# Kernel tuning notes

Hardware: AMD Instinct MI355X
Metric: run time of the kernel (lower is better)

The kernel has to match this reference:

```python
import jax, jax.numpy as jnp
import numpy as np

N_HEADS = 16
WINDOW = 256


def setup_inputs() -> dict:
    key = jax.random.key(0)
    ks = jax.random.split(key, 6)
    B, S, D = 2, 2048, 1024
    std = 0.02
    x = jax.random.normal(ks[0], (B, S, D), dtype=jnp.float32)
    wq = jax.random.normal(ks[1], (D, D), dtype=jnp.float32) * std
    wk = jax.random.normal(ks[2], (D, D), dtype=jnp.float32) * std
    wv = jax.random.normal(ks[3], (D, D), dtype=jnp.float32) * std
    wo = jax.random.normal(ks[4], (D, D), dtype=jnp.float32) * std
    bq = jnp.zeros((D,), jnp.float32)
    bk = jnp.zeros((D,), jnp.float32)
    bv = jnp.zeros((D,), jnp.float32)
    bo = jnp.zeros((D,), jnp.float32)
    return {"x": x, "wq": wq, "bq": bq, "wk": wk, "bk": bk,
            "wv": wv, "bv": bv, "wo": wo, "bo": bo}


def _sliding_window_bias(seq_len: int) -> jnp.ndarray:
    # allowed iff |i - j| <= WINDOW  ->  0.0, else -inf  (matches torch loop mask)
    i = jnp.arange(seq_len)[:, None]
    j = jnp.arange(seq_len)[None, :]
    allowed = jnp.abs(i - j) <= WINDOW
    return jnp.where(allowed, 0.0, -jnp.inf).astype(jnp.float32)


def reference(x, wq, bq, wk, bk, wv, bv, wo, bo):
    B, S, D = x.shape
    H = N_HEADS
    dh = D // H
    scale = dh ** -0.5
    # nn.Linear: y = x @ W^T + b
    q = (x @ wq.T + bq).reshape(B, S, H, dh).transpose(0, 2, 1, 3)  # [B,H,S,dh]
    k = (x @ wk.T + bk).reshape(B, S, H, dh).transpose(0, 2, 1, 3)
    v = (x @ wv.T + bv).reshape(B, S, H, dh).transpose(0, 2, 1, 3)
    scores = jnp.einsum('bhqd,bhkd->bhqk', q, k) * scale  # [B,H,S,S]
    scores = scores + _sliding_window_bias(S)[None, None]
    attn = jax.nn.softmax(scores, axis=-1)
    out = jnp.einsum('bhqk,bhkd->bhqd', attn, v)  # [B,H,S,dh]
    out = out.transpose(0, 2, 1, 3).reshape(B, S, D)
    return out @ wo.T + bo
```

## Files before the change

kernel.cpp:

```cpp
#include <hip/hip_runtime.h>
#include <stdint.h>

static constexpr int Ss = 2048;
static constexpr int Dd = 1024;
static constexpr int Hh = 16;
static constexpr int DH = 64;

typedef short bf16x8 __attribute__((ext_vector_type(8)));
typedef float f32x4 __attribute__((ext_vector_type(4)));

#define LOG2E 1.4426950408889634f

__device__ __forceinline__ uint16_t f2bf(float f) {
  uint32_t u = __builtin_bit_cast(uint32_t, f);
  u += 0x7fffu + ((u >> 16) & 1u);
  return (uint16_t)(u >> 16);
}
__device__ __forceinline__ float bf2f(uint16_t h) {
  uint32_t u = ((uint32_t)h) << 16;
  return __builtin_bit_cast(float, u);
}

template <int CTRL>
__device__ __forceinline__ float dppf(float x) {
  return __builtin_bit_cast(float,
      __builtin_amdgcn_update_dpp(0, __builtin_bit_cast(int, x), CTRL, 0xF, 0xF, true));
}
__device__ __forceinline__ float rowmax16(float v) {
  v = fmaxf(v, dppf<0x128>(v));
  v = fmaxf(v, dppf<0x124>(v));
  v = fmaxf(v, dppf<0x122>(v));
  v = fmaxf(v, dppf<0x121>(v));
  return v;
}
__device__ __forceinline__ float rowsum16(float v) {
  v += dppf<0x128>(v);
  v += dppf<0x124>(v);
  v += dppf<0x122>(v);
  v += dppf<0x121>(v);
  return v;
}
__device__ __forceinline__ float fexp2(float x) { return __builtin_amdgcn_exp2f(x); }

#define GAS(p) ((const __attribute__((address_space(1))) uint32_t*)(p))
#define LAS(p) ((__attribute__((address_space(3))) uint32_t*)(p))

__global__ void cvt_all(const float* __restrict__ x,
                        const float* __restrict__ w0, const float* __restrict__ w1,
                        const float* __restrict__ w2, const float* __restrict__ w3,
                        uint16_t* __restrict__ xb,
                        uint16_t* __restrict__ o0, uint16_t* __restrict__ o1,
                        uint16_t* __restrict__ o2, uint16_t* __restrict__ o3) {
  int bid = blockIdx.x;
  const float* in;
  uint16_t* out;
  int i;
  if (bid < 4096) {
    in = x; out = xb; i = bid * 256 + threadIdx.x;
  } else {
    int b2 = bid - 4096;
    int t = b2 >> 10;
    in = (t == 0) ? w0 : (t == 1) ? w1 : (t == 2) ? w2 : w3;
    out = (t == 0) ? o0 : (t == 1) ? o1 : (t == 2) ? o2 : o3;
    i = (b2 & 1023) * 256 + threadIdx.x;
  }
  float4 v = reinterpret_cast<const float4*>(in)[i];
  ushort4 o;
  o.x = f2bf(v.x); o.y = f2bf(v.y); o.z = f2bf(v.z); o.w = f2bf(v.w);
  reinterpret_cast<ushort4*>(out)[i] = o;
}

template <int MODE, int BN>
__global__ __launch_bounds__(256, 2) void gemm_nt(
    const uint16_t* __restrict__ A,
    const uint16_t* __restrict__ W0, const uint16_t* __restrict__ W1, const uint16_t* __restrict__ W2,
    const float* __restrict__ b0, const float* __restrict__ b1, const float* __restrict__ b2,
    void* __restrict__ O0, void* __restrict__ O1, void* __restrict__ O2,
    int M, int N, int K) {
  constexpr int NI = BN / 32;
  __shared__ __align__(16) uint8_t ldsA[128 * 128];
  __shared__ __align__(16) uint8_t ldsB[BN * 128];

  const int tid = threadIdx.x, w = tid >> 6, lane = tid & 63;
  const int q = lane & 15, g = lane >> 4;
  const int wm = w >> 1, wn = w & 1;
  const int bx = blockIdx.x, by = blockIdx.y, z = blockIdx.z;
  const uint16_t* Wp = (z == 0) ? W0 : (z == 1) ? W1 : W2;
  const float* bp = (z == 0) ? b0 : (z == 1) ? b1 : b2;
  void* Op = (z == 0) ? O0 : (z == 1) ? O1 : O2;

  f32x4 acc[4][NI] = {};

  const int nkt = K >> 6;
  for (int kt = 0; kt < nkt; ++kt) {
    const int k0 = kt << 6;
    __syncthreads();
#pragma unroll
    for (int i = 0; i < 4; ++i) {
      int Lb = w * 4096 + i * 1024 + lane * 16;
      int row = Lb >> 7, cb = Lb & 127;
      int col = (cb ^ ((row & 7) << 4)) >> 1;
      const uint16_t* srcA = A + (size_t)(bx * 128 + row) * K + k0 + col;
      __builtin_amdgcn_global_load_lds(GAS(srcA), LAS(ldsA + w * 4096 + i * 1024), 16, 0, 0);
    }
#pragma unroll
    for (int i = 0; i < BN / 32; ++i) {
      int Lb = w * (BN * 32) + i * 1024 + lane * 16;
      int row = Lb >> 7, cb = Lb & 127;
      int col = (cb ^ ((row & 7) << 4)) >> 1;
      const uint16_t* srcB = Wp + (size_t)(by * BN + row) * K + k0 + col;
      __builtin_amdgcn_global_load_lds(GAS(srcB), LAS(ldsB + w * (BN * 32) + i * 1024), 16, 0, 0);
    }
    __syncthreads();

    bf16x8 af[4][2], bfg[NI][2];
#pragma unroll
    for (int mi = 0; mi < 4; ++mi)
#pragma unroll
      for (int s = 0; s < 2; ++s) {
        int row = wm * 64 + mi * 16 + q;
        int cb = (16 * g + 64 * s) ^ ((row & 7) << 4);
        af[mi][s] = *(const bf16x8*)(ldsA + row * 128 + cb);
      }
#pragma unroll
    for (int ni = 0; ni < NI; ++ni)
#pragma unroll
      for (int s = 0; s < 2; ++s) {
        int row = wn * (BN / 2) + ni * 16 + q;
        int cb = (16 * g + 64 * s) ^ ((row & 7) << 4);
        bfg[ni][s] = *(const bf16x8*)(ldsB + row * 128 + cb);
      }
#pragma unroll
    for (int mi = 0; mi < 4; ++mi)
#pragma unroll
      for (int ni = 0; ni < NI; ++ni) {
        acc[mi][ni] = __builtin_amdgcn_mfma_f32_16x16x32_bf16(af[mi][0], bfg[ni][0], acc[mi][ni], 0, 0, 0);
        acc[mi][ni] = __builtin_amdgcn_mfma_f32_16x16x32_bf16(af[mi][1], bfg[ni][1], acc[mi][ni], 0, 0, 0);
      }
  }

  float bias[NI];
#pragma unroll
  for (int ni = 0; ni < NI; ++ni) bias[ni] = bp[by * BN + wn * (BN / 2) + ni * 16 + q];
#pragma unroll
  for (int mi = 0; mi < 4; ++mi)
#pragma unroll
    for (int ni = 0; ni < NI; ++ni)
#pragma unroll
      for (int r = 0; r < 4; ++r) {
        int m = bx * 128 + wm * 64 + mi * 16 + 4 * g + r;
        int n = by * BN + wn * (BN / 2) + ni * 16 + q;
        float v = acc[mi][ni][r] + bias[ni];
        if (MODE == 0) {
          int b = m >> 11, s = m & 2047, h = n >> 6, d = n & 63;
          ((uint16_t*)Op)[(((size_t)(b * Hh + h) * Ss + s) << 6) + d] = f2bf(v);
        } else {
          ((float*)Op)[(size_t)m * N + n] = v;
        }
      }
}

__global__ __launch_bounds__(256, 4) void attn_swa(
    const uint16_t* __restrict__ Qg, const uint16_t* __restrict__ Kg,
    const uint16_t* __restrict__ Vg, uint16_t* __restrict__ Og) {
  __shared__ __align__(16) uint8_t ldsK[2][64 * 128];
  __shared__ __align__(16) uint8_t ldsVt[2][64 * 128];
  __shared__ __align__(16) uint8_t ldsP[4][2048];

  const int tid = threadIdx.x, w = tid >> 6, lane = tid & 63;
  const int q = lane & 15, g = lane >> 4;
  const int qb = blockIdx.x, bh = blockIdx.y;
  const size_t hbase = (size_t)bh * Ss * DH;
  const uint16_t* Qp = Qg + hbase;
  const uint16_t* Kp = Kg + hbase;
  const uint16_t* Vp = Vg + hbase;
  const int q0 = qb * 64;
  const int qw = q0 + w * 16;

  bf16x8 aq[2];
#pragma unroll
  for (int s = 0; s < 2; ++s) {
    bf16x8 t = *(const bf16x8*)(Qp + (size_t)(qw + q) * DH + s * 32 + g * 8);
#pragma unroll
    for (int j = 0; j < 8; ++j) {
      float f = bf2f((uint16_t)t[j]) * 0.125f;
      t[j] = (short)f2bf(f);
    }
    aq[s] = t;
  }

  f32x4 accO[4] = {};
  float mrun[4] = {-1e30f, -1e30f, -1e30f, -1e30f};
  float lrun[4] = {0.f, 0.f, 0.f, 0.f};

  const int t0 = (q0 >= 256) ? (q0 - 256) : 0;
  const int t1 = (q0 + 320 <= Ss) ? (q0 + 320) : Ss;
  const int nt = (t1 - t0) >> 6;

#pragma unroll
  for (int i = 0; i < 2; ++i) {
    int Lb = w * 2048 + i * 1024 + lane * 16;
    int row = Lb >> 7, cb = Lb & 127;
    const uint16_t* srcK = Kp + (size_t)(t0 + row) * DH + ((cb ^ ((row & 7) << 4)) >> 1);
    __builtin_amdgcn_global_load_lds(GAS(srcK), LAS(ldsK[0] + w * 2048 + i * 1024), 16, 0, 0);
  }
  const uint16_t* vrow0 = Vp + (size_t)(t0 + lane) * DH + w * 16;
  bf16x8 v0 = *(const bf16x8*)(vrow0);
  bf16x8 v1 = *(const bf16x8*)(vrow0 + 8);

  for (int t = 0; t < nt; ++t) {
    const int kb0 = t0 + (t << 6);
    const int cur = t & 1, nxt = cur ^ 1;

    uint8_t* Vt = ldsVt[cur];
#pragma unroll
    for (int j = 0; j < 8; ++j) {
      int c0 = w * 16 + j;
      *(uint16_t*)(Vt + c0 * 128 + ((2 * lane) ^ ((c0 & 7) << 4))) = (uint16_t)v0[j];
      int c1 = w * 16 + 8 + j;
      *(uint16_t*)(Vt + c1 * 128 + ((2 * lane) ^ ((c1 & 7) << 4))) = (uint16_t)v1[j];
    }
    asm volatile("s_waitcnt lgkmcnt(0)" ::: "memory");
    __builtin_amdgcn_sched_barrier(0);
    __builtin_amdgcn_s_barrier();
    __builtin_amdgcn_sched_barrier(0);

    if (t + 1 < nt) {
#pragma unroll
      for (int i = 0; i < 2; ++i) {
        int Lb = w * 2048 + i * 1024 + lane * 16;
        int row = Lb >> 7, cb = Lb & 127;
        const uint16_t* srcK = Kp + (size_t)(kb0 + 64 + row) * DH + ((cb ^ ((row & 7) << 4)) >> 1);
        __builtin_amdgcn_global_load_lds(GAS(srcK), LAS(ldsK[nxt] + w * 2048 + i * 1024), 16, 0, 0);
      }
      const uint16_t* vrow = Vp + (size_t)(kb0 + 64 + lane) * DH + w * 16;
      v0 = *(const bf16x8*)(vrow);
      v1 = *(const bf16x8*)(vrow + 8);
    }

    const uint8_t* Kl = ldsK[cur];
    f32x4 sacc[4] = {};
#pragma unroll
    for (int kb = 0; kb < 4; ++kb) {
      int row = kb * 16 + q;
#pragma unroll
      for (int s = 0; s < 2; ++s) {
        int cb = (16 * g + 64 * s) ^ ((row & 7) << 4);
        bf16x8 bk = *(const bf16x8*)(Kl + row * 128 + cb);
        sacc[kb] = __builtin_amdgcn_mfma_f32_16x16x32_bf16(aq[s], bk, sacc[kb], 0, 0, 0);
      }
    }
    if (kb0 - q0 < -192 || kb0 - q0 > 192) {
#pragma unroll
      for (int kb = 0; kb < 4; ++kb) {
        int key = kb0 + kb * 16 + q;
#pragma unroll
        for (int r = 0; r < 4; ++r) {
          int qi = qw + 4 * g + r;
          int dd = qi - key;
          bool ok = (dd <= 256) && (dd >= -256);
          sacc[kb][r] = ok ? sacc[kb][r] : -1e30f;
        }
      }
    }
#pragma unroll
    for (int r = 0; r < 4; ++r) {
      float tm = fmaxf(fmaxf(sacc[0][r], sacc[1][r]), fmaxf(sacc[2][r], sacc[3][r]));
      tm = rowmax16(tm);
      float mnew = fmaxf(mrun[r], tm);
      float mL = mnew * LOG2E;
      float alpha = fexp2(__builtin_fmaf(mrun[r], LOG2E, -mL));
      mrun[r] = mnew;
      float p0 = fexp2(__builtin_fmaf(sacc[0][r], LOG2E, -mL));
      float p1 = fexp2(__builtin_fmaf(sacc[1][r], LOG2E, -mL));
      float p2 = fexp2(__builtin_fmaf(sacc[2][r], LOG2E, -mL));
      float p3 = fexp2(__builtin_fmaf(sacc[3][r], LOG2E, -mL));
      sacc[0][r] = p0; sacc[1][r] = p1; sacc[2][r] = p2; sacc[3][r] = p3;
      float rs = rowsum16((p0 + p1) + (p2 + p3));
      lrun[r] = lrun[r] * alpha + rs;
#pragma unroll
      for (int db = 0; db < 4; ++db) accO[db][r] *= alpha;
    }
    uint8_t* Pl = ldsP[w];
#pragma unroll
    for (int kb = 0; kb < 4; ++kb) {
      int col2 = (kb * 16 + q) * 2;
#pragma unroll
      for (int r = 0; r < 4; ++r) {
        int prow = 4 * g + r;
        *(uint16_t*)(Pl + prow * 128 + (col2 ^ ((prow & 7) << 4))) = f2bf(sacc[kb][r]);
      }
    }
    bf16x8 ap[2];
#pragma unroll
    for (int s = 0; s < 2; ++s) {
      int cb = (16 * g + 64 * s) ^ ((q & 7) << 4);
      ap[s] = *(const bf16x8*)(Pl + q * 128 + cb);
    }
#pragma unroll
    for (int db = 0; db < 4; ++db) {
      int vr = db * 16 + q;
#pragma unroll
      for (int s = 0; s < 2; ++s) {
        int cb = (64 * s + 16 * g) ^ ((vr & 7) << 4);
        bf16x8 bvf = *(const bf16x8*)(ldsVt[cur] + vr * 128 + cb);
        accO[db] = __builtin_amdgcn_mfma_f32_16x16x32_bf16(ap[s], bvf, accO[db], 0, 0, 0);
      }
    }
  }

  const int b2 = bh >> 4, h = bh & 15;
#pragma unroll
  for (int r = 0; r < 4; ++r) {
    float inv = 1.0f / lrun[r];
    int qi = qw + 4 * g + r;
    size_t rowbase = ((size_t)(b2 * Ss + qi)) * Dd + h * DH;
#pragma unroll
    for (int db = 0; db < 4; ++db) {
      Og[rowbase + db * 16 + q] = f2bf(accO[db][r] * inv);
    }
  }
}

extern "C" void kernel_launch(void* const* d_in, const int* in_sizes, int n_in,
                              void* d_out, int out_size, void* d_ws, size_t ws_size,
                              hipStream_t stream) {
  const float* x  = (const float*)d_in[0];
  const float* wq = (const float*)d_in[1];
  const float* bq = (const float*)d_in[2];
  const float* wk = (const float*)d_in[3];
  const float* bk = (const float*)d_in[4];
  const float* wv = (const float*)d_in[5];
  const float* bv = (const float*)d_in[6];
  const float* wo = (const float*)d_in[7];
  const float* bo = (const float*)d_in[8];
  float* out = (float*)d_out;

  uint8_t* ws = (uint8_t*)d_ws;
  uint16_t* xb  = (uint16_t*)(ws + (size_t)(0u  << 20));
  uint16_t* wqb = (uint16_t*)(ws + (size_t)(8u  << 20));
  uint16_t* wkb = (uint16_t*)(ws + (size_t)(10u << 20));
  uint16_t* wvb = (uint16_t*)(ws + (size_t)(12u << 20));
  uint16_t* wob = (uint16_t*)(ws + (size_t)(14u << 20));
  uint16_t* Qb  = (uint16_t*)(ws + (size_t)(16u << 20));
  uint16_t* Kb  = (uint16_t*)(ws + (size_t)(24u << 20));
  uint16_t* Vb  = (uint16_t*)(ws + (size_t)(32u << 20));
  uint16_t* AOb = (uint16_t*)(ws + (size_t)(40u << 20));

  cvt_all<<<8192, 256, 0, stream>>>(x, wq, wk, wv, wo, xb, wqb, wkb, wvb, wob);

  gemm_nt<0, 128><<<dim3(32, 8, 3), 256, 0, stream>>>(
      xb, wqb, wkb, wvb, bq, bk, bv, (void*)Qb, (void*)Kb, (void*)Vb, 4096, 1024, 1024);

  attn_swa<<<dim3(32, 32), 256, 0, stream>>>(Qb, Kb, Vb, AOb);

  gemm_nt<1, 64><<<dim3(32, 16, 1), 256, 0, stream>>>(
      AOb, wob, wob, wob, bo, bo, bo, (void*)out, (void*)out, (void*)out, 4096, 1024, 1024);
}
```

Baseline: 87.07 us.

## Widen attention blocks to 128 queries with 8 waves and per-wave tile skipping

The attention kernel now uses 512 threads (8 waves) per block covering 128 query rows, so each K/V tile loaded into LDS is shared by twice as many queries. Each wave now loads half as much K/V per tile. A per-wave bounds check skips the QK/softmax/PV work for key tiles that lie entirely outside that wave's sliding window, which the wider query span makes more frequent. The cost is half as many blocks (512 instead of 1024), more LDS per block, larger barriers, and extra divergence at the warp level. Launch bounds of 512 threads with 4 blocks per SM may also constrain registers.

```diff
diff --git a/kernel.cpp b/kernel.cpp
--- a/kernel.cpp
+++ b/kernel.cpp
@@ -160,12 +160,12 @@
       }
 }
 
-__global__ __launch_bounds__(256, 4) void attn_swa(
+__global__ __launch_bounds__(512, 4) void attn_swa(
     const uint16_t* __restrict__ Qg, const uint16_t* __restrict__ Kg,
     const uint16_t* __restrict__ Vg, uint16_t* __restrict__ Og) {
   __shared__ __align__(16) uint8_t ldsK[2][64 * 128];
   __shared__ __align__(16) uint8_t ldsVt[2][64 * 128];
-  __shared__ __align__(16) uint8_t ldsP[4][2048];
+  __shared__ __align__(16) uint8_t ldsP[8][2048];
 
   const int tid = threadIdx.x, w = tid >> 6, lane = tid & 63;
   const int q = lane & 15, g = lane >> 4;
@@ -174,7 +174,7 @@
   const uint16_t* Qp = Qg + hbase;
   const uint16_t* Kp = Kg + hbase;
   const uint16_t* Vp = Vg + hbase;
-  const int q0 = qb * 64;
+  const int q0 = qb * 128;
   const int qw = q0 + w * 16;
 
   bf16x8 aq[2];
@@ -194,31 +194,27 @@
   float lrun[4] = {0.f, 0.f, 0.f, 0.f};
 
   const int t0 = (q0 >= 256) ? (q0 - 256) : 0;
-  const int t1 = (q0 + 320 <= Ss) ? (q0 + 320) : Ss;
+  const int t1 = (q0 + 384 <= Ss) ? (q0 + 384) : Ss;
   const int nt = (t1 - t0) >> 6;
 
-#pragma unroll
-  for (int i = 0; i < 2; ++i) {
-    int Lb = w * 2048 + i * 1024 + lane * 16;
+  {
+    int Lb = w * 1024 + lane * 16;
     int row = Lb >> 7, cb = Lb & 127;
     const uint16_t* srcK = Kp + (size_t)(t0 + row) * DH + ((cb ^ ((row & 7) << 4)) >> 1);
-    __builtin_amdgcn_global_load_lds(GAS(srcK), LAS(ldsK[0] + w * 2048 + i * 1024), 16, 0, 0);
-  }
-  const uint16_t* vrow0 = Vp + (size_t)(t0 + lane) * DH + w * 16;
-  bf16x8 v0 = *(const bf16x8*)(vrow0);
-  bf16x8 v1 = *(const bf16x8*)(vrow0 + 8);
+    __builtin_amdgcn_global_load_lds(GAS(srcK), LAS(ldsK[0] + w * 1024), 16, 0, 0);
+  }
+  bf16x8 v0 = *(const bf16x8*)(Vp + (size_t)(t0 + lane) * DH + w * 8);
 
   for (int t = 0; t < nt; ++t) {
     const int kb0 = t0 + (t << 6);
     const int cur = t & 1, nxt = cur ^ 1;
 
+    asm volatile("s_waitcnt vmcnt(0)" ::: "memory");
     uint8_t* Vt = ldsVt[cur];
 #pragma unroll
     for (int j = 0; j < 8; ++j) {
-      int c0 = w * 16 + j;
-      *(uint16_t*)(Vt + c0 * 128 + ((2 * lane) ^ ((c0 & 7) << 4))) = (uint16_t)v0[j];
-      int c1 = w * 16 + 8 + j;
-      *(uint16_t*)(Vt + c1 * 128 + ((2 * lane) ^ ((c1 & 7) << 4))) = (uint16_t)v1[j];
+      int c = w * 8 + j;
+      *(uint16_t*)(Vt + c * 128 + ((2 * lane) ^ (j << 4))) = (uint16_t)v0[j];
     }
     asm volatile("s_waitcnt lgkmcnt(0)" ::: "memory");
     __builtin_amdgcn_sched_barrier(0);
@@ -226,85 +222,83 @@
     __builtin_amdgcn_sched_barrier(0);
 
     if (t + 1 < nt) {
-#pragma unroll
-      for (int i = 0; i < 2; ++i) {
-        int Lb = w * 2048 + i * 1024 + lane * 16;
-        int row = Lb >> 7, cb = Lb & 127;
-        const uint16_t* srcK = Kp + (size_t)(kb0 + 64 + row) * DH + ((cb ^ ((row & 7) << 4)) >> 1);
-        __builtin_amdgcn_global_load_lds(GAS(srcK), LAS(ldsK[nxt] + w * 2048 + i * 1024), 16, 0, 0);
-      }
-      const uint16_t* vrow = Vp + (size_t)(kb0 + 64 + lane) * DH + w * 16;
-      v0 = *(const bf16x8*)(vrow);
-      v1 = *(const bf16x8*)(vrow + 8);
-    }
-
-    const uint8_t* Kl = ldsK[cur];
-    f32x4 sacc[4] = {};
-#pragma unroll
-    for (int kb = 0; kb < 4; ++kb) {
-      int row = kb * 16 + q;
+      int Lb = w * 1024 + lane * 16;
+      int row = Lb >> 7, cb = Lb & 127;
+      const uint16_t* srcK = Kp + (size_t)(kb0 + 64 + row) * DH + ((cb ^ ((row & 7) << 4)) >> 1);
+      __builtin_amdgcn_global_load_lds(GAS(srcK), LAS(ldsK[nxt] + w * 1024), 16, 0, 0);
+      v0 = *(const bf16x8*)(Vp + (size_t)(kb0 + 64 + lane) * DH + w * 8);
+    }
+
+    const int dtile = kb0 - qw;
+    if (dtile >= -319 && dtile <= 271) {
+      const uint8_t* Kl = ldsK[cur];
+      f32x4 sacc[4] = {};
+#pragma unroll
+      for (int kb = 0; kb < 4; ++kb) {
+        int row = kb * 16 + q;
+#pragma unroll
+        for (int s = 0; s < 2; ++s) {
+          int cb = (16 * g + 64 * s) ^ ((row & 7) << 4);
+          bf16x8 bk = *(const bf16x8*)(Kl + row * 128 + cb);
+          sacc[kb] = __builtin_amdgcn_mfma_f32_16x16x32_bf16(aq[s], bk, sacc[kb], 0, 0, 0);
+        }
+      }
+      if (dtile < -192 || dtile > 192) {
+#pragma unroll
+        for (int kb = 0; kb < 4; ++kb) {
+          int key = kb0 + kb * 16 + q;
+#pragma unroll
+          for (int r = 0; r < 4; ++r) {
+            int qi = qw + 4 * g + r;
+            int dd = qi - key;
+            bool ok = (dd <= 256) && (dd >= -256);
+            sacc[kb][r] = ok ? sacc[kb][r] : -1e30f;
+          }
+        }
+      }
+#pragma unroll
+      for (int r = 0; r < 4; ++r) {
+        float tm = fmaxf(fmaxf(sacc[0][r], sacc[1][r]), fmaxf(sacc[2][r], sacc[3][r]));
+        tm = rowmax16(tm);
+        float mnew = fmaxf(mrun[r], tm);
+        float mL = mnew * LOG2E;
+        float alpha = fexp2(__builtin_fmaf(mrun[r], LOG2E, -mL));
+        mrun[r] = mnew;
+        float p0 = fexp2(__builtin_fmaf(sacc[0][r], LOG2E, -mL));
+        float p1 = fexp2(__builtin_fmaf(sacc[1][r], LOG2E, -mL));
+        float p2 = fexp2(__builtin_fmaf(sacc[2][r], LOG2E, -mL));
+        float p3 = fexp2(__builtin_fmaf(sacc[3][r], LOG2E, -mL));
+        sacc[0][r] = p0; sacc[1][r] = p1; sacc[2][r] = p2; sacc[3][r] = p3;
+        float rs = rowsum16((p0 + p1) + (p2 + p3));
+        lrun[r] = lrun[r] * alpha + rs;
+#pragma unroll
+        for (int db = 0; db < 4; ++db) accO[db][r] *= alpha;
+      }
+      uint8_t* Pl = ldsP[w];
+#pragma unroll
+      for (int kb = 0; kb < 4; ++kb) {
+        int col2 = (kb * 16 + q) * 2;
+#pragma unroll
+        for (int r = 0; r < 4; ++r) {
+          int prow = 4 * g + r;
+          *(uint16_t*)(Pl + prow * 128 + (col2 ^ ((prow & 7) << 4))) = f2bf(sacc[kb][r]);
+        }
+      }
+      bf16x8 ap[2];
 #pragma unroll
       for (int s = 0; s < 2; ++s) {
-        int cb = (16 * g + 64 * s) ^ ((row & 7) << 4);
-        bf16x8 bk = *(const bf16x8*)(Kl + row * 128 + cb);
-        sacc[kb] = __builtin_amdgcn_mfma_f32_16x16x32_bf16(aq[s], bk, sacc[kb], 0, 0, 0);
-      }
-    }
-    if (kb0 - q0 < -192 || kb0 - q0 > 192) {
-#pragma unroll
-      for (int kb = 0; kb < 4; ++kb) {
-        int key = kb0 + kb * 16 + q;
-#pragma unroll
-        for (int r = 0; r < 4; ++r) {
-          int qi = qw + 4 * g + r;
-          int dd = qi - key;
-          bool ok = (dd <= 256) && (dd >= -256);
-          sacc[kb][r] = ok ? sacc[kb][r] : -1e30f;
-        }
-      }
-    }
-#pragma unroll
-    for (int r = 0; r < 4; ++r) {
-      float tm = fmaxf(fmaxf(sacc[0][r], sacc[1][r]), fmaxf(sacc[2][r], sacc[3][r]));
-      tm = rowmax16(tm);
-      float mnew = fmaxf(mrun[r], tm);
-      float mL = mnew * LOG2E;
-      float alpha = fexp2(__builtin_fmaf(mrun[r], LOG2E, -mL));
-      mrun[r] = mnew;
-      float p0 = fexp2(__builtin_fmaf(sacc[0][r], LOG2E, -mL));
-      float p1 = fexp2(__builtin_fmaf(sacc[1][r], LOG2E, -mL));
-      float p2 = fexp2(__builtin_fmaf(sacc[2][r], LOG2E, -mL));
-      float p3 = fexp2(__builtin_fmaf(sacc[3][r], LOG2E, -mL));
-      sacc[0][r] = p0; sacc[1][r] = p1; sacc[2][r] = p2; sacc[3][r] = p3;
-      float rs = rowsum16((p0 + p1) + (p2 + p3));
-      lrun[r] = lrun[r] * alpha + rs;
-#pragma unroll
-      for (int db = 0; db < 4; ++db) accO[db][r] *= alpha;
-    }
-    uint8_t* Pl = ldsP[w];
-#pragma unroll
-    for (int kb = 0; kb < 4; ++kb) {
-      int col2 = (kb * 16 + q) * 2;
-#pragma unroll
-      for (int r = 0; r < 4; ++r) {
-        int prow = 4 * g + r;
-        *(uint16_t*)(Pl + prow * 128 + (col2 ^ ((prow & 7) << 4))) = f2bf(sacc[kb][r]);
-      }
-    }
-    bf16x8 ap[2];
-#pragma unroll
-    for (int s = 0; s < 2; ++s) {
-      int cb = (16 * g + 64 * s) ^ ((q & 7) << 4);
-      ap[s] = *(const bf16x8*)(Pl + q * 128 + cb);
-    }
-#pragma unroll
-    for (int db = 0; db < 4; ++db) {
-      int vr = db * 16 + q;
-#pragma unroll
-      for (int s = 0; s < 2; ++s) {
-        int cb = (64 * s + 16 * g) ^ ((vr & 7) << 4);
-        bf16x8 bvf = *(const bf16x8*)(ldsVt[cur] + vr * 128 + cb);
-        accO[db] = __builtin_amdgcn_mfma_f32_16x16x32_bf16(ap[s], bvf, accO[db], 0, 0, 0);
+        int cb = (16 * g + 64 * s) ^ ((q & 7) << 4);
+        ap[s] = *(const bf16x8*)(Pl + q * 128 + cb);
+      }
+#pragma unroll
+      for (int db = 0; db < 4; ++db) {
+        int vr = db * 16 + q;
+#pragma unroll
+        for (int s = 0; s < 2; ++s) {
+          int cb = (64 * s + 16 * g) ^ ((vr & 7) << 4);
+          bf16x8 bvf = *(const bf16x8*)(ldsVt[cur] + vr * 128 + cb);
+          accO[db] = __builtin_amdgcn_mfma_f32_16x16x32_bf16(ap[s], bvf, accO[db], 0, 0, 0);
+        }
       }
     }
   }
@@ -352,7 +346,7 @@
   gemm_nt<0, 128><<<dim3(32, 8, 3), 256, 0, stream>>>(
       xb, wqb, wkb, wvb, bq, bk, bv, (void*)Qb, (void*)Kb, (void*)Vb, 4096, 1024, 1024);
 
-  attn_swa<<<dim3(32, 32), 256, 0, stream>>>(Qb, Kb, Vb, AOb);
+  attn_swa<<<dim3(16, 32), 512, 0, stream>>>(Qb, Kb, Vb, AOb);
 
   gemm_nt<1, 64><<<dim3(32, 16, 1), 256, 0, stream>>>(
       AOb, wob, wob, wob, bo, bo, bo, (void*)out, (void*)out, (void*)out, 4096, 1024, 1024);
```

New measurement: 84.23 us. 3.3% less time.
